# Kernel optimization log

Hardware: AMD Instinct MI355X
Metric: run time of the kernel (lower is better)

Reference implementation:

```python
import jax, jax.numpy as jnp
import numpy as np

M, K = 3072, 768          # hardcoded in the torch module's forward
B, S = 8, 2048            # batch, sequence length
NNZ_PER_ROW = 230
NNZ = M * NNZ_PER_ROW


def setup_inputs() -> dict:
    key = jax.random.key(0)
    k1, k2, k3 = jax.random.split(key, 3)
    rng = np.random.default_rng(0)
    # unique, sorted column indices per row (valid CSR with fixed row nnz)
    cols = np.argsort(rng.random((M, K)), axis=1)[:, :NNZ_PER_ROW]
    cols = np.sort(cols, axis=1).astype(np.int32)
    column_indices = jnp.asarray(cols.reshape(-1))
    row_offsets = jnp.asarray((np.arange(M + 1) * NNZ_PER_ROW).astype(np.int32))
    # diffsort(row_offsets): rows sorted by nnz descending (all equal -> identity)
    row_indices = jnp.arange(M, dtype=jnp.int32)
    values = jax.random.normal(k1, (NNZ,), dtype=jnp.float32) * 0.02
    bias = jax.random.normal(k2, (M,), dtype=jnp.float32) * 0.02
    x = jax.random.normal(k3, (B, S, K), dtype=jnp.float32)
    return {"values": values, "bias": bias, "x": x,
            "row_indices": row_indices, "row_offsets": row_offsets,
            "column_indices": column_indices}


def reference(values, bias, x, row_indices, row_offsets, column_indices):
    # CSR [M, K] sparse weight times dense x: out = x @ W^T + bias
    # (left_spmm(m,k,...,x^T) gives [B, M, S]; .transpose(1,2) -> [B, S, M])
    nnz = values.shape[0]
    # row id of each nonzero from the CSR offsets
    row_ids = jnp.searchsorted(row_offsets, jnp.arange(nnz, dtype=row_offsets.dtype), side="right") - 1
    # scatter values into the (small) dense [M, K] weight; .add sums duplicates
    # exactly as SpMM accumulation would
    W = jnp.zeros((M, K), dtype=values.dtype).at[row_ids, column_indices].add(values)
    out = jnp.einsum("bsk,mk->bsm", x, W) + bias  # [B, S, M]
    return out
```

## Files before the change

kernel.cpp:

```cpp
#include <hip/hip_runtime.h>
#include <hip/hip_bf16.h>
#include <cstdint>

#define K_DIM 768
#define M_DIM 3072
#define BS_TOTAL 16384
#define BK 32
#define KT 24

typedef __attribute__((ext_vector_type(4))) float f32x4;
typedef __attribute__((ext_vector_type(8))) short bf16x8;
typedef __attribute__((ext_vector_type(4))) unsigned short u16x4;
typedef __attribute__((ext_vector_type(4))) float fv4;

typedef unsigned int u32_g __attribute__((address_space(1)));
typedef unsigned int u32_l __attribute__((address_space(3)));

static __device__ __forceinline__ void async_load16(const void* g, void* l) {
    __builtin_amdgcn_global_load_lds((const u32_g*)g, (u32_l*)l, 16, 0, 0);
}

#define BAR() __builtin_amdgcn_s_barrier()
#define SCHEDB() __builtin_amdgcn_sched_barrier(0)

static __device__ __forceinline__ unsigned short f2bf(float f) {
    unsigned u = __builtin_bit_cast(unsigned, f);
    u += 0x7fffu + ((u >> 16) & 1u);
    return (unsigned short)(u >> 16);
}

__global__ void prep_kernel(const float* __restrict__ values,
                            const int* __restrict__ row_offsets,
                            const int* __restrict__ column_indices,
                            unsigned short* __restrict__ Wb,
                            const float* __restrict__ x,
                            unsigned short* __restrict__ xb, int n4) {
    const int b = blockIdx.x;
    const int t = threadIdx.x;
    if (b < M_DIM) {
        const int r = b;
        unsigned int* wrow32 = (unsigned int*)(Wb + (size_t)r * K_DIM);
        for (int i = t; i < K_DIM / 2; i += 256) wrow32[i] = 0u;
        __syncthreads();
        const int start = row_offsets[r], end = row_offsets[r + 1];
        unsigned short* wrow = Wb + (size_t)r * K_DIM;
        for (int i = start + t; i < end; i += 256)
            wrow[column_indices[i]] = f2bf(values[i]);
    } else {
        const int i = (b - M_DIM) * 256 + t;
        if (i < n4) {
            fv4 v = ((const fv4*)x)[i];
            u16x4 o;
            o[0] = f2bf(v[0]); o[1] = f2bf(v[1]); o[2] = f2bf(v[2]); o[3] = f2bf(v[3]);
            ((u16x4*)xb)[i] = o;
        }
    }
}


#define STAGE_A(buf, t)                                                         \
    { _Pragma("unroll") for (int c = 0; c < 2; ++c) {                           \
        const int u = c * 512 + tid;                                            \
        const int row = u >> 2;                                                 \
        const int gs = (u & 3) ^ ((row >> 1) & 3);                              \
        async_load16(X + (size_t)(row0 + row) * K_DIM + (t) * BK + gs * 8,      \
                     &sm[buf][0][(size_t)u * 8]); } }

#define STAGE_B(buf, t)                                                         \
    { _Pragma("unroll") for (int c = 0; c < 2; ++c) {                           \
        const int u = c * 512 + tid;                                            \
        const int row = u >> 2;                                                 \
        const int gs = (u & 3) ^ ((row >> 1) & 3);                              \
        async_load16(W + (size_t)(col0 + row) * K_DIM + (t) * BK + gs * 8,      \
                     &sm[buf][1][(size_t)u * 8]); } }

#define LDA(buf)                                                                \
    { _Pragma("unroll") for (int mi = 0; mi < 8; ++mi) {                        \
        const int row = wm * 128 + mi * 16 + fr;                                \
        const int blk = kq ^ ((row >> 1) & 3);                                  \
        aq[mi] = *(const bf16x8*)&sm[buf][0][row * BK + blk * 8]; } }

#define LDB(buf)                                                                \
    { _Pragma("unroll") for (int ni = 0; ni < 4; ++ni) {                        \
        const int row = wn * 64 + ni * 16 + fr;                                 \
        const int blk = kq ^ ((row >> 1) & 3);                                  \
        bq[ni] = *(const bf16x8*)&sm[buf][1][row * BK + blk * 8]; } }

#define MFMA32()                                                                \
    { __builtin_amdgcn_s_setprio(1);                                            \
      _Pragma("unroll") for (int mi = 0; mi < 8; ++mi)                          \
      _Pragma("unroll") for (int ni = 0; ni < 4; ++ni)                          \
        acc[mi][ni] = __builtin_amdgcn_mfma_f32_16x16x32_bf16(                  \
            aq[mi], bq[ni], acc[mi][ni], 0, 0, 0);                              \
      __builtin_amdgcn_s_setprio(0); }

__global__ __launch_bounds__(512, 2) void gemm_kernel(
    const unsigned short* __restrict__ X,
    const unsigned short* __restrict__ W,
    const float* __restrict__ bias,
    float* __restrict__ out) {
    __shared__ __align__(16) unsigned short sm[2][2][256 * BK];

    const int bid = blockIdx.x;
    const int xcd = bid & 7;
    const int j   = bid >> 3;
    const int by  = xcd * 8 + (j & 7);
    const int bx  = j >> 3;
    const int row0 = by * 256;
    const int col0 = bx * 256;

    const int tid  = threadIdx.x;
    const int lane = tid & 63;
    const int wave = tid >> 6;
    const int wm = wave >> 2;
    const int wn = wave & 3;
    const int fr = lane & 15;
    const int kq = lane >> 4;

    f32x4 acc[8][4] = {};
    bf16x8 aq[8], bq[4];

    STAGE_A(0, 0); STAGE_B(0, 0);
    float bv[4];
#pragma unroll
    for (int ni = 0; ni < 4; ++ni) bv[ni] = bias[col0 + wn * 64 + ni * 16 + fr];
    asm volatile("s_waitcnt vmcnt(0)" ::: "memory");
    SCHEDB();
    BAR();

    for (int t = 0; t < KT; ++t) {
        const int buf = t & 1, nbuf = buf ^ 1;
        if (t + 1 < KT) { STAGE_A(nbuf, t + 1); STAGE_B(nbuf, t + 1); }
        LDA(buf);
        LDB(buf);
        MFMA32();
        if (t + 1 < KT) {
            asm volatile("s_waitcnt vmcnt(0)" ::: "memory");
            SCHEDB();
            BAR();
        }
    }

    const int orow0 = row0 + wm * 128 + kq * 4;
#pragma unroll
    for (int mi = 0; mi < 8; ++mi)
#pragma unroll
        for (int jj = 0; jj < 4; ++jj) {
            float* op = out + (size_t)(orow0 + mi * 16 + jj) * M_DIM + col0 + wn * 64 + fr;
#pragma unroll
            for (int ni = 0; ni < 4; ++ni)
                op[ni * 16] = acc[mi][ni][jj] + bv[ni];
        }
}

extern "C" void kernel_launch(void* const* d_in, const int* in_sizes, int n_in,
                              void* d_out, int out_size, void* d_ws, size_t ws_size,
                              hipStream_t stream) {
    const float* values         = (const float*)d_in[0];
    const float* bias           = (const float*)d_in[1];
    const float* x              = (const float*)d_in[2];
    const int*   row_offsets    = (const int*)d_in[4];
    const int*   column_indices = (const int*)d_in[5];

    unsigned short* Wb = (unsigned short*)d_ws;
    unsigned short* Xb = (unsigned short*)((char*)d_ws + (size_t)M_DIM * K_DIM * 2);

    const int n4 = BS_TOTAL * K_DIM / 4;
    const int prep_blocks = M_DIM + (n4 + 255) / 256;
    prep_kernel<<<prep_blocks, 256, 0, stream>>>(values, row_offsets, column_indices,
                                                 Wb, x, Xb, n4);

    const int grid = (BS_TOTAL / 256) * (M_DIM / 256);
    gemm_kernel<<<grid, 512, 0, stream>>>(Xb, Wb, bias, (float*)d_out);
}
```

Measured before the change: 112.3 us.

## Use 4 waves with 128x128 per-wave tiles and BK=64 with 8-way swizzle

Restructures the GEMM block from 8 waves of 128x64 warp tiles over BK=32 into 4 waves of 128x128 warp tiles over BK=64. The K-loop runs half as many iterations, so there are fewer barriers and a higher MFMA-to-LDS-read ratio per wave. The LDS XOR swizzle is widened to 8 groups to match the 64-element rows. The cost is a 64-entry f32x4 accumulator array (256 VGPRs) plus fragments, which forces one block per CU and lowers occupancy. LDS use doubles to 64KB, with more latency-hiding pressure on a single wavefront group.

After: 111.9 us. Within noise of the previous version (-0.3%).

```diff
diff --git a/kernel.cpp b/kernel.cpp
--- a/kernel.cpp
+++ b/kernel.cpp
@@ -5,8 +5,7 @@
 #define K_DIM 768
 #define M_DIM 3072
 #define BS_TOTAL 16384
-#define BK 32
-#define KT 24
+#define KT 12
 
 typedef __attribute__((ext_vector_type(4))) float f32x4;
 typedef __attribute__((ext_vector_type(8))) short bf16x8;
@@ -59,47 +58,27 @@
 
 
 #define STAGE_A(buf, t)                                                         \
-    { _Pragma("unroll") for (int c = 0; c < 2; ++c) {                           \
-        const int u = c * 512 + tid;                                            \
-        const int row = u >> 2;                                                 \
-        const int gs = (u & 3) ^ ((row >> 1) & 3);                              \
-        async_load16(X + (size_t)(row0 + row) * K_DIM + (t) * BK + gs * 8,      \
+    { _Pragma("unroll") for (int c = 0; c < 8; ++c) {                           \
+        const int u = c * 256 + tid;                                            \
+        const int row = u >> 3;                                                 \
+        const int gs = (u & 7) ^ (row & 7);                                     \
+        async_load16(X + (size_t)(row0 + row) * K_DIM + (t) * 64 + gs * 8,      \
                      &sm[buf][0][(size_t)u * 8]); } }
 
 #define STAGE_B(buf, t)                                                         \
-    { _Pragma("unroll") for (int c = 0; c < 2; ++c) {                           \
-        const int u = c * 512 + tid;                                            \
-        const int row = u >> 2;                                                 \
-        const int gs = (u & 3) ^ ((row >> 1) & 3);                              \
-        async_load16(W + (size_t)(col0 + row) * K_DIM + (t) * BK + gs * 8,      \
+    { _Pragma("unroll") for (int c = 0; c < 8; ++c) {                           \
+        const int u = c * 256 + tid;                                            \
+        const int row = u >> 3;                                                 \
+        const int gs = (u & 7) ^ (row & 7);                                     \
+        async_load16(W + (size_t)(col0 + row) * K_DIM + (t) * 64 + gs * 8,      \
                      &sm[buf][1][(size_t)u * 8]); } }
 
-#define LDA(buf)                                                                \
-    { _Pragma("unroll") for (int mi = 0; mi < 8; ++mi) {                        \
-        const int row = wm * 128 + mi * 16 + fr;                                \
-        const int blk = kq ^ ((row >> 1) & 3);                                  \
-        aq[mi] = *(const bf16x8*)&sm[buf][0][row * BK + blk * 8]; } }
-
-#define LDB(buf)                                                                \
-    { _Pragma("unroll") for (int ni = 0; ni < 4; ++ni) {                        \
-        const int row = wn * 64 + ni * 16 + fr;                                 \
-        const int blk = kq ^ ((row >> 1) & 3);                                  \
-        bq[ni] = *(const bf16x8*)&sm[buf][1][row * BK + blk * 8]; } }
-
-#define MFMA32()                                                                \
-    { __builtin_amdgcn_s_setprio(1);                                            \
-      _Pragma("unroll") for (int mi = 0; mi < 8; ++mi)                          \
-      _Pragma("unroll") for (int ni = 0; ni < 4; ++ni)                          \
-        acc[mi][ni] = __builtin_amdgcn_mfma_f32_16x16x32_bf16(                  \
-            aq[mi], bq[ni], acc[mi][ni], 0, 0, 0);                              \
-      __builtin_amdgcn_s_setprio(0); }
-
-__global__ __launch_bounds__(512, 2) void gemm_kernel(
+__global__ __launch_bounds__(256, 1) void gemm_kernel(
     const unsigned short* __restrict__ X,
     const unsigned short* __restrict__ W,
     const float* __restrict__ bias,
     float* __restrict__ out) {
-    __shared__ __align__(16) unsigned short sm[2][2][256 * BK];
+    __shared__ __align__(16) unsigned short sm[2][2][256 * 64];
 
     const int bid = blockIdx.x;
     const int xcd = bid & 7;
@@ -112,18 +91,18 @@
     const int tid  = threadIdx.x;
     const int lane = tid & 63;
     const int wave = tid >> 6;
-    const int wm = wave >> 2;
-    const int wn = wave & 3;
+    const int wm = wave >> 1;
+    const int wn = wave & 1;
     const int fr = lane & 15;
     const int kq = lane >> 4;
 
-    f32x4 acc[8][4] = {};
-    bf16x8 aq[8], bq[4];
+    f32x4 acc[8][8] = {};
+
+    float bv[8];
+#pragma unroll
+    for (int ni = 0; ni < 8; ++ni) bv[ni] = bias[col0 + wn * 128 + ni * 16 + fr];
 
     STAGE_A(0, 0); STAGE_B(0, 0);
-    float bv[4];
-#pragma unroll
-    for (int ni = 0; ni < 4; ++ni) bv[ni] = bias[col0 + wn * 64 + ni * 16 + fr];
     asm volatile("s_waitcnt vmcnt(0)" ::: "memory");
     SCHEDB();
     BAR();
@@ -131,9 +110,32 @@
     for (int t = 0; t < KT; ++t) {
         const int buf = t & 1, nbuf = buf ^ 1;
         if (t + 1 < KT) { STAGE_A(nbuf, t + 1); STAGE_B(nbuf, t + 1); }
-        LDA(buf);
-        LDB(buf);
-        MFMA32();
+
+#pragma unroll
+        for (int ks = 0; ks < 2; ++ks) {
+            bf16x8 aq[8], bq[8];
+#pragma unroll
+            for (int mi = 0; mi < 8; ++mi) {
+                const int row = wm * 128 + mi * 16 + fr;
+                const int g = (ks * 4 + kq) ^ (row & 7);
+                aq[mi] = *(const bf16x8*)&sm[buf][0][row * 64 + g * 8];
+            }
+#pragma unroll
+            for (int ni = 0; ni < 8; ++ni) {
+                const int row = wn * 128 + ni * 16 + fr;
+                const int g = (ks * 4 + kq) ^ (row & 7);
+                bq[ni] = *(const bf16x8*)&sm[buf][1][row * 64 + g * 8];
+            }
+            __builtin_amdgcn_s_setprio(1);
+#pragma unroll
+            for (int mi = 0; mi < 8; ++mi)
+#pragma unroll
+                for (int ni = 0; ni < 8; ++ni)
+                    acc[mi][ni] = __builtin_amdgcn_mfma_f32_16x16x32_bf16(
+                        aq[mi], bq[ni], acc[mi][ni], 0, 0, 0);
+            __builtin_amdgcn_s_setprio(0);
+        }
+
         if (t + 1 < KT) {
             asm volatile("s_waitcnt vmcnt(0)" ::: "memory");
             SCHEDB();
@@ -146,9 +148,10 @@
     for (int mi = 0; mi < 8; ++mi)
 #pragma unroll
         for (int jj = 0; jj < 4; ++jj) {
-            float* op = out + (size_t)(orow0 + mi * 16 + jj) * M_DIM + col0 + wn * 64 + fr;
+            float* op = out + (size_t)(orow0 + mi * 16 + jj) * M_DIM
+                        + col0 + wn * 128 + fr;
 #pragma unroll
-            for (int ni = 0; ni < 4; ++ni)
+            for (int ni = 0; ni < 8; ++ni)
                 op[ni * 16] = acc[mi][ni][jj] + bv[ni];
         }
 }
@@ -171,5 +174,5 @@
                                                  Wb, x, Xb, n4);
 
     const int grid = (BS_TOTAL / 256) * (M_DIM / 256);
-    gemm_kernel<<<grid, 512, 0, stream>>>(Xb, Wb, bias, (float*)d_out);
+    gemm_kernel<<<grid, 256, 0, stream>>>(Xb, Wb, bias, (float*)d_out);
 }
```
